# Performance work log

Measured on AMD Instinct MI355X. Metric: run time of the kernel, lower is better.

The kernel has to match this reference:

```python
import jax, jax.numpy as jnp
import numpy as np

EMBED_DIM = 1024
NUM_HEADS = 16
HEAD_DIM = EMBED_DIM // NUM_HEADS  # 64
GRID_H, GRID_W = 24, 24
BASE = 10000.0


def rope2d_cache(head_dim=HEAD_DIM, grid_h=GRID_H, grid_w=GRID_W, base=BASE):
    # "Concatenated Embeddings" 2D RoPE cache -> (cos, sin), each [grid_h*grid_w, head_dim]
    pos_dim = head_dim // 2
    inv_freq = 1.0 / (base ** (jnp.arange(0, pos_dim, 2, dtype=jnp.float32) / pos_dim))
    max_grid = max(grid_h, grid_w)
    positions = jnp.arange(max_grid, dtype=jnp.float32)
    freqs = positions[:, None] * inv_freq[None, :]            # [max_grid, pos_dim//2]
    emb_1d = jnp.concatenate([freqs, freqs], axis=-1)          # [max_grid, pos_dim]
    h_emb = jnp.broadcast_to(emb_1d[:grid_h, None, :], (grid_h, grid_w, pos_dim))
    w_emb = jnp.broadcast_to(emb_1d[None, :grid_w, :], (grid_h, grid_w, pos_dim))
    emb_2d = jnp.concatenate([h_emb, w_emb], axis=-1).reshape(-1, head_dim)
    return jnp.cos(emb_2d), jnp.sin(emb_2d)


def rotate_half(x):
    x1, x2 = jnp.split(x, 2, axis=-1)
    return jnp.concatenate([-x2, x1], axis=-1)


def setup_inputs() -> dict:
    key = jax.random.key(0)
    ks = jax.random.split(key, 9)
    B, S, E = 16, GRID_H * GRID_W + 1, EMBED_DIM
    s = 1.0 / np.sqrt(E)
    inp = {
        "hidden_states": jax.random.normal(ks[0], (B, S, E), dtype=jnp.float32),
        "Wq": jax.random.normal(ks[1], (E, E), dtype=jnp.float32) * s,
        "bq": jnp.zeros((E,), dtype=jnp.float32),
        "Wk": jax.random.normal(ks[2], (E, E), dtype=jnp.float32) * s,
        "bk": jnp.zeros((E,), dtype=jnp.float32),
        "Wv": jax.random.normal(ks[3], (E, E), dtype=jnp.float32) * s,
        "bv": jnp.zeros((E,), dtype=jnp.float32),
        "Wo": jax.random.normal(ks[4], (E, E), dtype=jnp.float32) * s,
        "bo": jnp.zeros((E,), dtype=jnp.float32),
    }
    return inp


def reference(hidden_states, Wq, bq, Wk, bk, Wv, bv, Wo, bo):
    B, S, E = hidden_states.shape
    H, D = NUM_HEADS, HEAD_DIM
    scale = D ** -0.5

    def proj(W, b):
        # torch Linear: x @ W.T + b; reshape to [B, H, S, D]
        y = jnp.einsum('bse,fe->bsf', hidden_states, W) + b
        return y.reshape(B, S, H, D).transpose(0, 2, 1, 3)

    q = proj(Wq, bq)
    k = proj(Wk, bk)
    v = proj(Wv, bv)

    cos, sin = rope2d_cache()                 # [num_patches, D]
    cos = cos[None, None, :, :]
    sin = sin[None, None, :, :]

    # CLS token at position 0 is untouched; RoPE applied to patch tokens 1:
    qp = q[:, :, 1:, :]
    kp = k[:, :, 1:, :]
    qp = qp * cos + rotate_half(qp) * sin
    kp = kp * cos + rotate_half(kp) * sin
    q = jnp.concatenate([q[:, :, :1, :], qp], axis=2)
    k = jnp.concatenate([k[:, :, :1, :], kp], axis=2)

    scores = jnp.einsum('bhqd,bhkd->bhqk', q, k) * scale   # [B,H,S,S]
    attn = jax.nn.softmax(scores, axis=-1)
    out = jnp.einsum('bhqk,bhkd->bhqd', attn, v)           # [B,H,S,D]
    out = out.transpose(0, 2, 1, 3).reshape(B, S, E)
    out = jnp.einsum('bse,fe->bsf', out, Wo) + bo
    return out
```

## Files before the change

kernel.cpp:

```cpp
#include <hip/hip_runtime.h>
#include <hip/hip_bf16.h>
#include <stdint.h>

typedef __bf16 bf16_t;
typedef __attribute__((ext_vector_type(4))) float floatx4;
typedef __attribute__((ext_vector_type(8))) __bf16 bf16x8;
typedef __attribute__((ext_vector_type(4))) __bf16 bf16x4;

#define MFMA16(a, b, c) __builtin_amdgcn_mfma_f32_16x16x32_bf16(a, b, c, 0, 0, 0)

#define GLOAD_LDS16(gsrc, ldst)                                                          \
  __builtin_amdgcn_global_load_lds((const __attribute__((address_space(1))) void*)(gsrc),\
                                   (__attribute__((address_space(3))) void*)(ldst),      \
                                   16, 0, 0)

#define BATCH 16
#define SEQ   577
#define EMB   1024
#define NH    16
#define HD    64
#define SPAD  640
#define MROWS (BATCH * SEQ)
#define MPAD  9344

#define EXP_C 0.1803368801111404f

#define OFF_H  0ULL
#define OFF_WQ 19136512ULL
#define OFF_WK 21233664ULL
#define OFF_WV 23330816ULL
#define OFF_WO 25427968ULL
#define OFF_Q  27525120ULL
#define OFF_K  48496640ULL
#define OFF_VT 69468160ULL
#define OFF_AO 90439680ULL

__global__ __launch_bounds__(256) void k_cast(
    const float4* __restrict__ hs, const float4* __restrict__ wq,
    const float4* __restrict__ wk, const float4* __restrict__ wv,
    const float4* __restrict__ wo, bf16x4* __restrict__ hb, bf16x4* __restrict__ wqb,
    bf16x4* __restrict__ wkb, bf16x4* __restrict__ wvb, bf16x4* __restrict__ wob) {
  int idx = blockIdx.x * 256 + threadIdx.x;
  const int H4 = MROWS * EMB / 4;
  const int W4 = EMB * EMB / 4;
  const float4* src;
  bf16x4* dst;
  int i;
  if (idx < H4) {
    src = hs; dst = hb; i = idx;
  } else {
    int r = idx - H4;
    int w = r / W4;
    if (w >= 4) return;
    i = r - w * W4;
    src = (w == 0) ? wq : (w == 1) ? wk : (w == 2) ? wv : wo;
    dst = (w == 0) ? wqb : (w == 1) ? wkb : (w == 2) ? wvb : wob;
  }
  float4 v = src[i];
  bf16x4 o;
  o.x = (bf16_t)v.x; o.y = (bf16_t)v.y; o.z = (bf16_t)v.z; o.w = (bf16_t)v.w;
  dst[i] = o;
}

__global__ __launch_bounds__(256, 3) void k_qkv(const bf16_t* __restrict__ A,
                                                const bf16_t* __restrict__ Wq,
                                                const bf16_t* __restrict__ Wk,
                                                const bf16_t* __restrict__ Wv,
                                                const float* __restrict__ bq,
                                                const float* __restrict__ bk,
                                                const float* __restrict__ bv,
                                                bf16_t* __restrict__ qb,
                                                bf16_t* __restrict__ kb,
                                                bf16_t* __restrict__ vtb) {
  __shared__ bf16_t As[128 * 32];
  __shared__ bf16_t Bs[3 * 64 * 32];
  const int hh = blockIdx.x;
  const int n0 = hh * 64;
  const int m0 = blockIdx.y * 128;
  const int t = threadIdx.x;
  const int wid = t >> 6, lane = t & 63, quad = lane >> 4, c = lane & 15;

  floatx4 acc[3][2][4];
#pragma unroll
  for (int z = 0; z < 3; z++)
#pragma unroll
    for (int i = 0; i < 2; i++)
#pragma unroll
      for (int j = 0; j < 4; j++) {
        floatx4 zz = {0.f, 0.f, 0.f, 0.f};
        acc[z][i][j] = zz;
      }

  for (int k0 = 0; k0 < EMB; k0 += 32) {
    __syncthreads();
#pragma unroll
    for (int i = 0; i < 2; i++) {
      int ci = i * 256 + t;
      int row = ci >> 2, off = (ci & 3) * 8;
      GLOAD_LDS16(A + (size_t)(m0 + row) * EMB + k0 + off, (char*)As + (i * 256 + wid * 64) * 16);
    }
    {
      int row = t >> 2, off = (t & 3) * 8;
      GLOAD_LDS16(Wq + (size_t)(n0 + row) * EMB + k0 + off, (char*)Bs + (wid * 64) * 16);
      GLOAD_LDS16(Wk + (size_t)(n0 + row) * EMB + k0 + off, (char*)Bs + 4096 + (wid * 64) * 16);
      GLOAD_LDS16(Wv + (size_t)(n0 + row) * EMB + k0 + off, (char*)Bs + 8192 + (wid * 64) * 16);
    }
    __syncthreads();
    bf16x8 af[2];
#pragma unroll
    for (int mi = 0; mi < 2; mi++)
      af[mi] = *(const bf16x8*)(As + (wid * 32 + mi * 16 + c) * 32 + quad * 8);
#pragma unroll
    for (int z = 0; z < 3; z++) {
      bf16x8 bfr[4];
#pragma unroll
      for (int ni = 0; ni < 4; ni++)
        bfr[ni] = *(const bf16x8*)(Bs + z * 2048 + (ni * 16 + c) * 32 + quad * 8);
#pragma unroll
      for (int mi = 0; mi < 2; mi++)
#pragma unroll
        for (int ni = 0; ni < 4; ni++) acc[z][mi][ni] = MFMA16(af[mi], bfr[ni], acc[z][mi][ni]);
    }
  }

  const float invf = exp2f(-(float)c * 0.8304820237218405f);

  for (int z = 0; z < 3; z++) {
    const float* bias = (z == 0) ? bq : (z == 1) ? bk : bv;
    float bias_v[4];
#pragma unroll
    for (int ni = 0; ni < 4; ni++) bias_v[ni] = bias[n0 + ni * 16 + c];
#pragma unroll
    for (int mi = 0; mi < 2; mi++) {
#pragma unroll
      for (int r = 0; r < 4; r++) {
        int m = m0 + wid * 32 + mi * 16 + quad * 4 + r;
        if (m >= MROWS) continue;
        int bb = m / SEQ;
        int s = m - bb * SEQ;
        if (z < 2) {
          float ch = 1.f, sh = 0.f, cw = 1.f, sw = 0.f;
          if (s > 0) {
            int p = s - 1;
            int hp = p / 24, wp = p - (p / 24) * 24;
            __sincosf((float)hp * invf, &sh, &ch);
            __sincosf((float)wp * invf, &sw, &cw);
          }
          bf16_t* dst = (z == 0) ? qb : kb;
          size_t rowoff = ((size_t)(bb * NH + hh) * SPAD + s) * HD;
#pragma unroll
          for (int ni = 0; ni < 4; ni++) {
            float val = acc[z][mi][ni][r] + bias_v[ni];
            float part = acc[z][mi][ni ^ 2][r] + bias_v[ni ^ 2];
            float rot = (ni < 2) ? -part : part;
            float cs = (ni < 2) ? ch : cw;
            float sn = (ni < 2) ? sh : sw;
            dst[rowoff + ni * 16 + c] = (bf16_t)(val * cs + rot * sn);
          }
        } else {
          size_t base = (size_t)(bb * NH + hh) * HD;
#pragma unroll
          for (int ni = 0; ni < 4; ni++) {
            float val = acc[z][mi][ni][r] + bias_v[ni];
            int d = ni * 16 + c;
            vtb[(base + d) * SPAD + s] = (bf16_t)val;
          }
        }
      }
    }
  }
}

#define PSTR 72
#define OSTR 66
__global__ __launch_bounds__(256, 4) void k_attn(const bf16_t* __restrict__ qb,
                                                 const bf16_t* __restrict__ kb,
                                                 const bf16_t* __restrict__ vtb,
                                                 bf16_t* __restrict__ ao) {
  __shared__ bf16_t Ks[64 * PSTR];
  __shared__ bf16_t Vs[64 * PSTR];
  __shared__ bf16_t Ps[4 * 32 * PSTR];
  const int t = threadIdx.x, wid = t >> 6, lane = t & 63, quad = lane >> 4, c = lane & 15;
  const int hh = blockIdx.x, bb = blockIdx.y, qt = blockIdx.z;
  const size_t bh = (size_t)bb * NH + hh;
  const bf16_t* qbase = qb + bh * SPAD * HD + (size_t)qt * 128 * HD;
  const bf16_t* kbase = kb + bh * SPAD * HD;
  const bf16_t* vbase = vtb + bh * HD * SPAD;

  bf16x8 aq[2][2];
#pragma unroll
  for (int mi = 0; mi < 2; mi++)
#pragma unroll
    for (int h = 0; h < 2; h++)
      aq[mi][h] = *(const bf16x8*)(qbase + (size_t)(wid * 32 + mi * 16 + c) * HD + h * 32 + quad * 8);

  uint4 kr[2], vr[2];
#pragma unroll
  for (int j = 0; j < 2; j++) {
    int ci = j * 256 + t;
    int row = ci >> 3, off = (ci & 7) * 8;
    kr[j] = *(const uint4*)(kbase + (size_t)row * HD + off);
    vr[j] = *(const uint4*)(vbase + (size_t)row * SPAD + off);
  }

  bf16x8 ones;
#pragma unroll
  for (int i = 0; i < 8; i++) ones[i] = (bf16_t)1.0f;

  floatx4 acc_o[2][4], acc_l[2];
#pragma unroll
  for (int mi = 0; mi < 2; mi++) {
    floatx4 z = {0.f, 0.f, 0.f, 0.f};
    acc_l[mi] = z;
#pragma unroll
    for (int nd = 0; nd < 4; nd++) acc_o[mi][nd] = z;
  }

  bf16_t* Pw = Ps + wid * 32 * PSTR;

  for (int kt = 0; kt < 9; kt++) {
    __syncthreads();
#pragma unroll
    for (int j = 0; j < 2; j++) {
      int ci = j * 256 + t;
      int row = ci >> 3, off = (ci & 7) * 8;
      *(uint4*)((char*)Ks + (row * PSTR + off) * 2) = kr[j];
      *(uint4*)((char*)Vs + (row * PSTR + off) * 2) = vr[j];
    }
    __syncthreads();
    if (kt < 8) {
#pragma unroll
      for (int j = 0; j < 2; j++) {
        int ci = j * 256 + t;
        int row = ci >> 3, off = (ci & 7) * 8;
        kr[j] = *(const uint4*)(kbase + (size_t)((kt + 1) * 64 + row) * HD + off);
        vr[j] = *(const uint4*)(vbase + (size_t)row * SPAD + (kt + 1) * 64 + off);
      }
    }

    floatx4 sc[2][4];
#pragma unroll
    for (int ni = 0; ni < 4; ni++) {
      bf16x8 k0 = *(const bf16x8*)(Ks + (ni * 16 + c) * PSTR + quad * 8);
      bf16x8 k1 = *(const bf16x8*)(Ks + (ni * 16 + c) * PSTR + 32 + quad * 8);
#pragma unroll
      for (int mi = 0; mi < 2; mi++) {
        floatx4 zz = {0.f, 0.f, 0.f, 0.f};
        zz = MFMA16(aq[mi][0], k0, zz);
        zz = MFMA16(aq[mi][1], k1, zz);
        sc[mi][ni] = zz;
      }
    }
#pragma unroll
    for (int mi = 0; mi < 2; mi++)
#pragma unroll
      for (int ni = 0; ni < 4; ni++)
#pragma unroll
        for (int r = 0; r < 4; r++) {
          float p = exp2f(sc[mi][ni][r] * EXP_C);
          Pw[(mi * 16 + quad * 4 + r) * PSTR + ni * 16 + c] = (bf16_t)p;
        }
    bf16x8 pa[2][2];
#pragma unroll
    for (int mi = 0; mi < 2; mi++)
#pragma unroll
      for (int h = 0; h < 2; h++)
        pa[mi][h] = *(const bf16x8*)(Pw + (mi * 16 + c) * PSTR + h * 32 + quad * 8);
#pragma unroll
    for (int nd = 0; nd < 4; nd++) {
      bf16x8 v0 = *(const bf16x8*)(Vs + (nd * 16 + c) * PSTR + quad * 8);
      bf16x8 v1 = *(const bf16x8*)(Vs + (nd * 16 + c) * PSTR + 32 + quad * 8);
#pragma unroll
      for (int mi = 0; mi < 2; mi++) {
        acc_o[mi][nd] = MFMA16(pa[mi][0], v0, acc_o[mi][nd]);
        acc_o[mi][nd] = MFMA16(pa[mi][1], v1, acc_o[mi][nd]);
      }
    }
#pragma unroll
    for (int mi = 0; mi < 2; mi++) {
      acc_l[mi] = MFMA16(pa[mi][0], ones, acc_l[mi]);
      acc_l[mi] = MFMA16(pa[mi][1], ones, acc_l[mi]);
    }
  }

  {
    bf16x8 klast[2];
#pragma unroll
    for (int h = 0; h < 2; h++) {
      bf16x8 kk;
#pragma unroll
      for (int i = 0; i < 8; i++) kk[i] = (bf16_t)0.0f;
      if (c == 0) kk = *(const bf16x8*)(kbase + (size_t)576 * HD + h * 32 + quad * 8);
      klast[h] = kk;
    }
    float vlast[4];
#pragma unroll
    for (int nd = 0; nd < 4; nd++)
      vlast[nd] = (float)vbase[(size_t)(nd * 16 + c) * SPAD + 576];
#pragma unroll
    for (int mi = 0; mi < 2; mi++) {
      floatx4 zz = {0.f, 0.f, 0.f, 0.f};
      zz = MFMA16(aq[mi][0], klast[0], zz);
      zz = MFMA16(aq[mi][1], klast[1], zz);
#pragma unroll
      for (int r = 0; r < 4; r++) {
        float p = exp2f(zz[r] * EXP_C);
        p = __shfl(p, quad * 16, 64);
#pragma unroll
        for (int nd = 0; nd < 4; nd++) acc_o[mi][nd][r] += p * vlast[nd];
        acc_l[mi][r] += p;
      }
    }
  }

  {
#pragma unroll
    for (int mi = 0; mi < 2; mi++)
#pragma unroll
      for (int r = 0; r < 4; r++) {
        float inv_l = 1.f / acc_l[mi][r];
        int row = mi * 16 + quad * 4 + r;
#pragma unroll
        for (int nd = 0; nd < 4; nd++)
          Pw[row * OSTR + nd * 16 + c] = (bf16_t)(acc_o[mi][nd][r] * inv_l);
      }
    const int rsub = lane >> 3, c8 = lane & 7;
#pragma unroll
    for (int j = 0; j < 4; j++) {
      int row = j * 8 + rsub;
      bf16x8 ov = *(const bf16x8*)(Pw + row * OSTR + c8 * 8);
      int q = qt * 128 + wid * 32 + row;
      if (q < SEQ) {
        size_t mrow = (size_t)bb * SEQ + q;
        *(bf16x8*)(ao + mrow * EMB + hh * HD + c8 * 8) = ov;
      }
    }
  }
}

__global__ __launch_bounds__(256) void k_oproj(const bf16_t* __restrict__ A,
                                               const bf16_t* __restrict__ Wo,
                                               const float* __restrict__ bo,
                                               float* __restrict__ out) {
  __shared__ bf16_t As[128 * 32];
  __shared__ bf16_t Bs[128 * 32];
  const int n0 = blockIdx.x * 128, m0 = blockIdx.y * 128;
  const int t = threadIdx.x;
  const int wid = t >> 6, lane = t & 63, quad = lane >> 4, c = lane & 15;
  const int wr = wid >> 1, wc = wid & 1;
  floatx4 acc[4][4];
#pragma unroll
  for (int i = 0; i < 4; i++)
#pragma unroll
    for (int j = 0; j < 4; j++) {
      floatx4 z = {0.f, 0.f, 0.f, 0.f};
      acc[i][j] = z;
    }
  for (int k0 = 0; k0 < EMB; k0 += 32) {
    __syncthreads();
#pragma unroll
    for (int i = 0; i < 2; i++) {
      int ci = i * 256 + t;
      int row = ci >> 2, off = (ci & 3) * 8;
      GLOAD_LDS16(A + (size_t)(m0 + row) * EMB + k0 + off, (char*)As + (i * 256 + wid * 64) * 16);
      GLOAD_LDS16(Wo + (size_t)(n0 + row) * EMB + k0 + off, (char*)Bs + (i * 256 + wid * 64) * 16);
    }
    __syncthreads();
    bf16x8 af[4], bfr[4];
#pragma unroll
    for (int mi = 0; mi < 4; mi++)
      af[mi] = *(const bf16x8*)(As + (wr * 64 + mi * 16 + c) * 32 + quad * 8);
#pragma unroll
    for (int ni = 0; ni < 4; ni++)
      bfr[ni] = *(const bf16x8*)(Bs + (wc * 64 + ni * 16 + c) * 32 + quad * 8);
#pragma unroll
    for (int mi = 0; mi < 4; mi++)
#pragma unroll
      for (int ni = 0; ni < 4; ni++) acc[mi][ni] = MFMA16(af[mi], bfr[ni], acc[mi][ni]);
  }
  float bias_v[4];
#pragma unroll
  for (int ni = 0; ni < 4; ni++) bias_v[ni] = bo[n0 + wc * 64 + ni * 16 + c];
#pragma unroll
  for (int mi = 0; mi < 4; mi++)
#pragma unroll
    for (int r = 0; r < 4; r++) {
      int m = m0 + wr * 64 + mi * 16 + quad * 4 + r;
      if (m >= MROWS) continue;
#pragma unroll
      for (int ni = 0; ni < 4; ni++)
        out[(size_t)m * EMB + n0 + wc * 64 + ni * 16 + c] = acc[mi][ni][r] + bias_v[ni];
    }
}

extern "C" void kernel_launch(void* const* d_in, const int* in_sizes, int n_in, void* d_out,
                              int out_size, void* d_ws, size_t ws_size, hipStream_t stream) {
  const float* hs = (const float*)d_in[0];
  const float* Wq = (const float*)d_in[1];
  const float* bq = (const float*)d_in[2];
  const float* Wk = (const float*)d_in[3];
  const float* bk = (const float*)d_in[4];
  const float* Wv = (const float*)d_in[5];
  const float* bv = (const float*)d_in[6];
  const float* Wo = (const float*)d_in[7];
  const float* bo = (const float*)d_in[8];
  float* out = (float*)d_out;
  char* ws = (char*)d_ws;

  bf16_t* hb = (bf16_t*)(ws + OFF_H);
  bf16_t* wqb = (bf16_t*)(ws + OFF_WQ);
  bf16_t* wkb = (bf16_t*)(ws + OFF_WK);
  bf16_t* wvb = (bf16_t*)(ws + OFF_WV);
  bf16_t* wob = (bf16_t*)(ws + OFF_WO);
  bf16_t* qbuf = (bf16_t*)(ws + OFF_Q);
  bf16_t* kbuf = (bf16_t*)(ws + OFF_K);
  bf16_t* vtbuf = (bf16_t*)(ws + OFF_VT);
  bf16_t* aob = (bf16_t*)(ws + OFF_AO);


  k_cast<<<13328, 256, 0, stream>>>((const float4*)hs, (const float4*)Wq, (const float4*)Wk,
                                    (const float4*)Wv, (const float4*)Wo, (bf16x4*)hb,
                                    (bf16x4*)wqb, (bf16x4*)wkb, (bf16x4*)wvb, (bf16x4*)wob);

  dim3 gq(16, 73);
  k_qkv<<<gq, 256, 0, stream>>>(hb, wqb, wkb, wvb, bq, bk, bv, qbuf, kbuf, vtbuf);

  dim3 ga(16, 16, 5);
  k_attn<<<ga, 256, 0, stream>>>(qbuf, kbuf, vtbuf, aob);

  dim3 go(8, 73);
  k_oproj<<<go, 256, 0, stream>>>(aob, wob, bo, out);
}
```

Baseline: 330.7 us.

## Enlarge attention query tile to 192 rows and handle last query separately

Each attention block now covers 192 query rows (48 per wave) instead of 128, so the grid drops from 5 to 3 query tiles per head. This removes the padded fifth tile and lets each block reuse the K/V tiles it stages across more query rows. Query row 576, which the 3x192 tiling leaves out, is computed by the qt==2 block using a scalar dot-product and reduction path. In exchange, registers and LDS per block grow, the launch-bounds occupancy target drops from 4 to 3, and the grid is smaller and has a serial tail.

```diff
diff --git a/kernel.cpp b/kernel.cpp
--- a/kernel.cpp
+++ b/kernel.cpp
@@ -173,26 +173,28 @@
 
 #define PSTR 72
 #define OSTR 66
-__global__ __launch_bounds__(256, 4) void k_attn(const bf16_t* __restrict__ qb,
+#define MI   3
+__global__ __launch_bounds__(256, 3) void k_attn(const bf16_t* __restrict__ qb,
                                                  const bf16_t* __restrict__ kb,
                                                  const bf16_t* __restrict__ vtb,
                                                  bf16_t* __restrict__ ao) {
   __shared__ bf16_t Ks[64 * PSTR];
   __shared__ bf16_t Vs[64 * PSTR];
-  __shared__ bf16_t Ps[4 * 32 * PSTR];
+  __shared__ bf16_t Ps[4 * 48 * PSTR];
   const int t = threadIdx.x, wid = t >> 6, lane = t & 63, quad = lane >> 4, c = lane & 15;
   const int hh = blockIdx.x, bb = blockIdx.y, qt = blockIdx.z;
   const size_t bh = (size_t)bb * NH + hh;
-  const bf16_t* qbase = qb + bh * SPAD * HD + (size_t)qt * 128 * HD;
+  const bf16_t* qall = qb + bh * SPAD * HD;
+  const bf16_t* qbase = qall + (size_t)qt * 192 * HD;
   const bf16_t* kbase = kb + bh * SPAD * HD;
   const bf16_t* vbase = vtb + bh * HD * SPAD;
 
-  bf16x8 aq[2][2];
-#pragma unroll
-  for (int mi = 0; mi < 2; mi++)
+  bf16x8 aq[MI][2];
+#pragma unroll
+  for (int mi = 0; mi < MI; mi++)
 #pragma unroll
     for (int h = 0; h < 2; h++)
-      aq[mi][h] = *(const bf16x8*)(qbase + (size_t)(wid * 32 + mi * 16 + c) * HD + h * 32 + quad * 8);
+      aq[mi][h] = *(const bf16x8*)(qbase + (size_t)(wid * 48 + mi * 16 + c) * HD + h * 32 + quad * 8);
 
   uint4 kr[2], vr[2];
 #pragma unroll
@@ -207,16 +209,16 @@
 #pragma unroll
   for (int i = 0; i < 8; i++) ones[i] = (bf16_t)1.0f;
 
-  floatx4 acc_o[2][4], acc_l[2];
-#pragma unroll
-  for (int mi = 0; mi < 2; mi++) {
+  floatx4 acc_o[MI][4], acc_l[MI];
+#pragma unroll
+  for (int mi = 0; mi < MI; mi++) {
     floatx4 z = {0.f, 0.f, 0.f, 0.f};
     acc_l[mi] = z;
 #pragma unroll
     for (int nd = 0; nd < 4; nd++) acc_o[mi][nd] = z;
   }
 
-  bf16_t* Pw = Ps + wid * 32 * PSTR;
+  bf16_t* Pw = Ps + wid * 48 * PSTR;
 
   for (int kt = 0; kt < 9; kt++) {
     __syncthreads();
@@ -238,13 +240,13 @@
       }
     }
 
-    floatx4 sc[2][4];
+    floatx4 sc[MI][4];
 #pragma unroll
     for (int ni = 0; ni < 4; ni++) {
       bf16x8 k0 = *(const bf16x8*)(Ks + (ni * 16 + c) * PSTR + quad * 8);
       bf16x8 k1 = *(const bf16x8*)(Ks + (ni * 16 + c) * PSTR + 32 + quad * 8);
 #pragma unroll
-      for (int mi = 0; mi < 2; mi++) {
+      for (int mi = 0; mi < MI; mi++) {
         floatx4 zz = {0.f, 0.f, 0.f, 0.f};
         zz = MFMA16(aq[mi][0], k0, zz);
         zz = MFMA16(aq[mi][1], k1, zz);
@@ -252,7 +254,7 @@
       }
     }
 #pragma unroll
-    for (int mi = 0; mi < 2; mi++)
+    for (int mi = 0; mi < MI; mi++)
 #pragma unroll
       for (int ni = 0; ni < 4; ni++)
 #pragma unroll
@@ -260,9 +262,9 @@
           float p = exp2f(sc[mi][ni][r] * EXP_C);
           Pw[(mi * 16 + quad * 4 + r) * PSTR + ni * 16 + c] = (bf16_t)p;
         }
-    bf16x8 pa[2][2];
-#pragma unroll
-    for (int mi = 0; mi < 2; mi++)
+    bf16x8 pa[MI][2];
+#pragma unroll
+    for (int mi = 0; mi < MI; mi++)
 #pragma unroll
       for (int h = 0; h < 2; h++)
         pa[mi][h] = *(const bf16x8*)(Pw + (mi * 16 + c) * PSTR + h * 32 + quad * 8);
@@ -271,13 +273,13 @@
       bf16x8 v0 = *(const bf16x8*)(Vs + (nd * 16 + c) * PSTR + quad * 8);
       bf16x8 v1 = *(const bf16x8*)(Vs + (nd * 16 + c) * PSTR + 32 + quad * 8);
 #pragma unroll
-      for (int mi = 0; mi < 2; mi++) {
+      for (int mi = 0; mi < MI; mi++) {
         acc_o[mi][nd] = MFMA16(pa[mi][0], v0, acc_o[mi][nd]);
         acc_o[mi][nd] = MFMA16(pa[mi][1], v1, acc_o[mi][nd]);
       }
     }
 #pragma unroll
-    for (int mi = 0; mi < 2; mi++) {
+    for (int mi = 0; mi < MI; mi++) {
       acc_l[mi] = MFMA16(pa[mi][0], ones, acc_l[mi]);
       acc_l[mi] = MFMA16(pa[mi][1], ones, acc_l[mi]);
     }
@@ -298,7 +300,7 @@
     for (int nd = 0; nd < 4; nd++)
       vlast[nd] = (float)vbase[(size_t)(nd * 16 + c) * SPAD + 576];
 #pragma unroll
-    for (int mi = 0; mi < 2; mi++) {
+    for (int mi = 0; mi < MI; mi++) {
       floatx4 zz = {0.f, 0.f, 0.f, 0.f};
       zz = MFMA16(aq[mi][0], klast[0], zz);
       zz = MFMA16(aq[mi][1], klast[1], zz);
@@ -315,7 +317,7 @@
 
   {
 #pragma unroll
-    for (int mi = 0; mi < 2; mi++)
+    for (int mi = 0; mi < MI; mi++)
 #pragma unroll
       for (int r = 0; r < 4; r++) {
         float inv_l = 1.f / acc_l[mi][r];
@@ -326,14 +328,55 @@
       }
     const int rsub = lane >> 3, c8 = lane & 7;
 #pragma unroll
-    for (int j = 0; j < 4; j++) {
+    for (int j = 0; j < 6; j++) {
       int row = j * 8 + rsub;
       bf16x8 ov = *(const bf16x8*)(Pw + row * OSTR + c8 * 8);
-      int q = qt * 128 + wid * 32 + row;
-      if (q < SEQ) {
-        size_t mrow = (size_t)bb * SEQ + q;
-        *(bf16x8*)(ao + mrow * EMB + hh * HD + c8 * 8) = ov;
-      }
+      int q = qt * 192 + wid * 48 + row;
+      size_t mrow = (size_t)bb * SEQ + q;
+      *(bf16x8*)(ao + mrow * EMB + hh * HD + c8 * 8) = ov;
+    }
+  }
+
+  if (qt == 2) {
+    float* Pt = (float*)Ks;
+    float* Ot = Pt + 584;
+    __syncthreads();
+    bf16x8 qv8[8];
+    const bf16_t* q576 = qall + (size_t)576 * HD;
+#pragma unroll
+    for (int ch = 0; ch < 8; ch++) qv8[ch] = *(const bf16x8*)(q576 + ch * 8);
+#pragma unroll
+    for (int rep = 0; rep < 3; rep++) {
+      int j = t + rep * 256;
+      if (j < SEQ) {
+        const bf16_t* krow = kbase + (size_t)j * HD;
+        float s = 0.f;
+#pragma unroll
+        for (int ch = 0; ch < 8; ch++) {
+          bf16x8 kx = *(const bf16x8*)(krow + ch * 8);
+#pragma unroll
+          for (int e = 0; e < 8; e++) s += (float)qv8[ch][e] * (float)kx[e];
+        }
+        Pt[j] = exp2f(s * EXP_C);
+      }
+    }
+    __syncthreads();
+    {
+      int d = t & 63, g = t >> 6;
+      int j0 = g * 145, j1 = (g == 3) ? SEQ : (j0 + 145);
+      const bf16_t* vrow = vbase + (size_t)d * SPAD;
+      float o = 0.f;
+      for (int j = j0; j < j1; j++) o += Pt[j] * (float)vrow[j];
+      Ot[g * 64 + d] = o;
+    }
+    __syncthreads();
+    if (wid == 0) {
+      float l = 0.f;
+      for (int k2 = lane; k2 < SEQ; k2 += 64) l += Pt[k2];
+#pragma unroll
+      for (int off = 1; off < 64; off <<= 1) l += __shfl_xor(l, off, 64);
+      float sum = Ot[lane] + Ot[64 + lane] + Ot[128 + lane] + Ot[192 + lane];
+      ao[((size_t)bb * SEQ + 576) * EMB + hh * HD + lane] = (bf16_t)(sum / l);
     }
   }
 }
@@ -425,7 +468,7 @@
   dim3 gq(16, 73);
   k_qkv<<<gq, 256, 0, stream>>>(hb, wqb, wkb, wvb, bq, bk, bv, qbuf, kbuf, vtbuf);
 
-  dim3 ga(16, 16, 5);
+  dim3 ga(16, 16, 3);
   k_attn<<<ga, 256, 0, stream>>>(qbuf, kbuf, vtbuf, aob);
 
   dim3 go(8, 73);
```

After: 374.4 us. +13.2%, slower.
